# Kernel tuning notes

Measured on AMD Instinct MI355X. Metric: run time of the kernel, lower is better.

Reference implementation:

```python
import jax, jax.numpy as jnp
import numpy as np
from jax import lax

DILATIONS = [1, 2, 4, 8, 16, 32, 64, 128, 256, 512]
KERNEL = 3
CH = 64
B, T = 8, 16384
L = len(DILATIONS)


def setup_inputs() -> dict:
    key = jax.random.key(0)
    ks = jax.random.split(key, 5)
    x = jax.random.normal(ks[0], (B, CH, T), dtype=jnp.float32)
    # gated conv: out_channels = 2*CH (tanh half | sigmoid half)
    weights_conv = jax.random.normal(ks[1], (L, 2 * CH, CH, KERNEL), dtype=jnp.float32) * 0.1
    biases_conv = jax.random.normal(ks[2], (L, 2 * CH), dtype=jnp.float32) * 0.1
    weights_out = jax.random.normal(ks[3], (L, CH, CH), dtype=jnp.float32) * 0.1
    biases_out = jax.random.normal(ks[4], (L, CH), dtype=jnp.float32) * 0.1
    return {
        "x": x,
        "weights_conv": weights_conv,
        "biases_conv": biases_conv,
        "weights_out": weights_out,
        "biases_out": biases_out,
    }


def _stack_forward(x, weights_conv, biases_conv, weights_out, biases_out):
    skips = []
    for i, d in enumerate(DILATIONS):
        h = x  # residual branch
        pad = (KERNEL - 1) * d  # causal left padding
        y = lax.conv_general_dilated(
            x, weights_conv[i],
            window_strides=(1,), padding=[(pad, 0)], rhs_dilation=(d,),
            dimension_numbers=("NCH", "OIH", "NCH"),
        ) + biases_conv[i][None, :, None]
        yt, ys = jnp.split(y, 2, axis=1)          # gated activation
        a = jnp.tanh(yt) * jax.nn.sigmoid(ys)      # (B, CH, T)
        skips.append(a)                            # skip = activation output
        if i < L - 1:  # last layer has use_output_transform=False
            out = jnp.einsum("oc,bct->bot", weights_out[i], a) + biases_out[i][None, :, None]
        else:
            out = a
        x = out + h  # residual add
    # pack (output, skips[0..L-1]) into one array of shape (L+1, B, CH, T)
    return jnp.concatenate([x[None], jnp.stack(skips, axis=0)], axis=0)


def reference(x, weights_conv, biases_conv, weights_out, biases_out):
    return _stack_forward(x, weights_conv, biases_conv, weights_out, biases_out)
```

## Files before the change

kernel.cpp:

```cpp
#include <hip/hip_runtime.h>
#include <hip/hip_bf16.h>


#define CH 64
#define TLEN 16384
#define NB 8
#define BN 128
#define NLAYER 10

typedef __attribute__((ext_vector_type(4))) float f32x4;
typedef __attribute__((ext_vector_type(8))) short s16x8;
typedef __attribute__((ext_vector_type(4))) unsigned short u16x4;

__device__ __forceinline__ unsigned short f2bf(float f) {
    union { float f; unsigned u; } v; v.f = f;
    unsigned r = v.u + 0x7fffu + ((v.u >> 16) & 1u);
    return (unsigned short)(r >> 16);
}
__device__ __forceinline__ float bf2f(unsigned short u) {
    union { unsigned u; float f; } v; v.u = ((unsigned)u) << 16;
    return v.f;
}
__device__ __forceinline__ void gload_lds16(const void* g, void* l) {
    __builtin_amdgcn_global_load_lds(
        (const __attribute__((address_space(1))) unsigned int*)g,
        (__attribute__((address_space(3))) unsigned int*)l, 16, 0, 0);
}

#define NCONV (NLAYER * 4 * 2 * 6 * 64 * 8)
#define NOUT  (NLAYER * 4 * 2 * 64 * 8)

__global__ void pack_weights(const float* __restrict__ wconv,
                             const float* __restrict__ wout,
                             unsigned short* __restrict__ wcpk,
                             unsigned short* __restrict__ wopk)
{
    int idx = blockIdx.x * 256 + threadIdx.x;
    if (idx < NCONV) {
        int j = idx & 7, t = idx >> 3;
        int lane = t & 63; t >>= 6;
        int ks = t % 6;   t /= 6;
        int m  = t & 1;   t >>= 1;
        int wv = t & 3;   int l = t >> 2;
        int o  = (m * 4 + wv) * 16 + (lane & 15);
        int ck = ks * 32 + (lane >> 4) * 8 + j;
        int kk = ck >> 6, c = ck & 63;
        wcpk[idx] = f2bf(wconv[(((size_t)l * 128 + o) * CH + c) * 3 + (2 - kk)]);
    } else if (idx < NCONV + NOUT) {
        int id = idx - NCONV;
        int j = id & 7, t = id >> 3;
        int lane = t & 63; t >>= 6;
        int ks = t & 1;    t >>= 1;
        int wv = t & 3;    int l = t >> 2;
        int o  = wv * 16 + (lane & 15);
        int c  = ks * 32 + (lane >> 4) * 8 + j;
        wopk[id] = f2bf(wout[((size_t)l * CH + o) * CH + c]);
    }
}

template<int I0, bool SRC_F32>
__global__ __launch_bounds__(256, 4)
void wavenet_pair(const void* __restrict__ xin_,
                  unsigned short* __restrict__ xoutp,
                  float* __restrict__ out,
                  const unsigned short* __restrict__ wcpk,
                  const unsigned short* __restrict__ wopk,
                  const float* __restrict__ bconv,
                  const float* __restrict__ bout)
{
    constexpr int d   = 1 << I0;
    constexpr int D   = 2 * d;
    constexpr int TD  = 2 * D;
    constexpr int W1T = (128 + TD + 15) / 16;
    constexpr int W1  = W1T * 16;
    constexpr int WIN = W1 + 2 * d;

    __shared__ __align__(16) unsigned short xs[WIN * 64];
    __shared__ __align__(16) unsigned short ci[W1 * 64];
    __shared__ __align__(16) unsigned short as2[64 * 64];

    const int tid  = threadIdx.x;
    const int lane = tid & 63;
    const int wv   = tid >> 6;
    const int hrow = lane & 15;
    const int kgrp = lane >> 4;
    const int b  = blockIdx.y;
    const int t0 = blockIdx.x * BN;
    const size_t xbase  = (size_t)b * CH * TLEN;
    const size_t planeF = (size_t)NB * CH * TLEN;
    const int o0 = wv * 16 + kgrp * 4;
    const int lo = t0 - 6 * d;

    if (SRC_F32) {
        const float* x = (const float*)xin_;
        #pragma unroll
        for (int c8 = 0; c8 < 8; ++c8) {
            for (int p = tid; p < WIN; p += 256) {
                const int tt = lo + p;
                s16x8 pk = {0, 0, 0, 0, 0, 0, 0, 0};
                if (tt >= 0 && tt < TLEN) {
                    const float* pp = x + xbase + (size_t)(c8 * 8) * TLEN + tt;
                    #pragma unroll
                    for (int j = 0; j < 8; ++j) pk[j] = (short)f2bf(pp[(size_t)j * TLEN]);
                }
                *reinterpret_cast<s16x8*>(&xs[(size_t)(c8 * WIN + p) * 8]) = pk;
            }
        }
    } else {
        const unsigned short* xb = (const unsigned short*)xin_ + xbase;
        constexpr int cnt = (WIN + 63) / 64;
        if (lo >= 0 && lo + WIN <= TLEN) {
            for (int task = wv; task < 8 * cnt; task += 4) {
                const int c8 = task / cnt, n0 = (task % cnt) * 64;
                const int rem = WIN - n0;
                const unsigned short* sp = xb + (size_t)(lo + n0 + lane) * CH + c8 * 8;
                unsigned short* dp = &xs[(size_t)(c8 * WIN + n0) * 8];
                if (rem >= 64) gload_lds16(sp, dp);
                else if (lane < rem) gload_lds16(sp, dp);
            }
        } else {
            for (int task = wv; task < 8 * cnt; task += 4) {
                const int c8 = task / cnt, n0 = (task % cnt) * 64;
                const int p = n0 + lane;
                if (p < WIN) {
                    const int tt = lo + p;
                    s16x8 pk = {0, 0, 0, 0, 0, 0, 0, 0};
                    if (tt >= 0 && tt < TLEN)
                        pk = *reinterpret_cast<const s16x8*>(xb + (size_t)tt * CH + c8 * 8);
                    *reinterpret_cast<s16x8*>(&xs[(size_t)(c8 * WIN + p) * 8]) = pk;
                }
            }
        }
    }

    s16x8 w0[6], w1[6], wa2[2];
    float bt[4], bs[4], bo[4];
    auto loadw = [&](int L) {
        const unsigned short* bw = wcpk + ((size_t)(L * 4 + wv) * 768 + lane) * 8;
        #pragma unroll
        for (int ks = 0; ks < 6; ++ks) {
            w0[ks] = *reinterpret_cast<const s16x8*>(bw + (size_t)ks * 512);
            w1[ks] = *reinterpret_cast<const s16x8*>(bw + (size_t)(6 + ks) * 512);
        }
        const unsigned short* b2 = wopk + ((size_t)(L * 4 + wv) * 128 + lane) * 8;
        wa2[0] = *reinterpret_cast<const s16x8*>(b2);
        wa2[1] = *reinterpret_cast<const s16x8*>(b2 + 512);
        const float* Bc = bconv + (size_t)L * 128;
        const float* Bo = bout + (size_t)L * CH;
        #pragma unroll
        for (int r = 0; r < 4; ++r) {
            bt[r] = Bc[o0 + r];
            bs[r] = Bc[64 + o0 + r];
            bo[r] = Bo[o0 + r];
        }
    };

    loadw(I0);
    __syncthreads();

    float* skipA = out + (size_t)(1 + I0) * planeF + xbase;
    #pragma unroll 1
    for (int c0 = 0; c0 < W1T; c0 += 3) {
        f32x4 aT[3], aS[3];
        #pragma unroll
        for (int i3 = 0; i3 < 3; ++i3) {
            aT[i3] = (f32x4){0.f, 0.f, 0.f, 0.f};
            aS[i3] = (f32x4){0.f, 0.f, 0.f, 0.f};
        }
        #pragma unroll
        for (int i3 = 0; i3 < 3; ++i3) {
            const int q = (c0 + i3) * 16 + hrow;
            #pragma unroll
            for (int ks = 0; ks < 6; ++ks) {
                const int kb = ks * 4 + kgrp;
                const int kk = kb >> 3, c8i = kb & 7;
                const s16x8 bf = *reinterpret_cast<const s16x8*>(
                    &xs[(size_t)(c8i * WIN + q + (2 - kk) * d) * 8]);
                aT[i3] = __builtin_amdgcn_mfma_f32_16x16x32_bf16(w0[ks], bf, aT[i3], 0, 0, 0);
                aS[i3] = __builtin_amdgcn_mfma_f32_16x16x32_bf16(w1[ks], bf, aS[i3], 0, 0, 0);
            }
        }
        #pragma unroll
        for (int i3 = 0; i3 < 3; ++i3) {
            const int q = (c0 + i3) * 16 + hrow;
            #pragma unroll
            for (int r = 0; r < 4; ++r) {
                const float yt = aT[i3][r] + bt[r];
                const float ys = aS[i3][r] + bs[r];
                const float th = 2.f * __builtin_amdgcn_rcpf(1.f + __expf(-2.f * yt)) - 1.f;
                const float sg = __builtin_amdgcn_rcpf(1.f + __expf(-ys));
                const float av = th * sg;
                const int c = o0 + r;
                if (q >= TD && q < TD + 128)
                    __builtin_nontemporal_store(av, &skipA[(size_t)c * TLEN + t0 + q - TD]);
                ci[(size_t)((c >> 3) * W1 + q) * 8 + (c & 7)] = f2bf(av);
            }
        }
        __syncthreads();
        u16x4 stash[3];
        #pragma unroll
        for (int i3 = 0; i3 < 3; ++i3) {
            const int q = (c0 + i3) * 16 + hrow;
            f32x4 acc = (f32x4){0.f, 0.f, 0.f, 0.f};
            #pragma unroll
            for (int ks2 = 0; ks2 < 2; ++ks2) {
                const s16x8 bf = *reinterpret_cast<const s16x8*>(
                    &ci[(size_t)((ks2 * 4 + kgrp) * W1 + q) * 8]);
                acc = __builtin_amdgcn_mfma_f32_16x16x32_bf16(wa2[ks2], bf, acc, 0, 0, 0);
            }
            const u16x4 rv = *reinterpret_cast<const u16x4*>(
                &xs[(size_t)((o0 >> 3) * WIN + q + 2 * d) * 8 + (o0 & 7)]);
            u16x4 ov;
            #pragma unroll
            for (int r = 0; r < 4; ++r)
                ov[r] = (t0 + q >= TD) ? f2bf(acc[r] + bo[r] + bf2f(rv[r]))
                                       : (unsigned short)0;
            stash[i3] = ov;
        }
        __syncthreads();
        #pragma unroll
        for (int i3 = 0; i3 < 3; ++i3) {
            const int q = (c0 + i3) * 16 + hrow;
            *reinterpret_cast<u16x4*>(&ci[(size_t)((o0 >> 3) * W1 + q) * 8 + (o0 & 7)]) = stash[i3];
        }
    }
    __syncthreads();

    loadw(I0 + 1);
    float* skipB = out + (size_t)(2 + I0) * planeF + xbase;
    unsigned short* xo = xoutp + xbase;

    #pragma unroll 1
    for (int hf = 0; hf < 2; ++hf) {
        f32x4 aT[4], aS[4];
        #pragma unroll
        for (int i4 = 0; i4 < 4; ++i4) {
            aT[i4] = (f32x4){0.f, 0.f, 0.f, 0.f};
            aS[i4] = (f32x4){0.f, 0.f, 0.f, 0.f};
        }
        #pragma unroll
        for (int i4 = 0; i4 < 4; ++i4) {
            const int n = (hf * 4 + i4) * 16 + hrow;
            #pragma unroll
            for (int ks = 0; ks < 6; ++ks) {
                const int kb = ks * 4 + kgrp;
                const int kk = kb >> 3, c8i = kb & 7;
                const s16x8 bf = *reinterpret_cast<const s16x8*>(
                    &ci[(size_t)(c8i * W1 + n + (2 - kk) * D) * 8]);
                aT[i4] = __builtin_amdgcn_mfma_f32_16x16x32_bf16(w0[ks], bf, aT[i4], 0, 0, 0);
                aS[i4] = __builtin_amdgcn_mfma_f32_16x16x32_bf16(w1[ks], bf, aS[i4], 0, 0, 0);
            }
        }
        #pragma unroll
        for (int i4 = 0; i4 < 4; ++i4) {
            const int n = (hf * 4 + i4) * 16 + hrow;
            #pragma unroll
            for (int r = 0; r < 4; ++r) {
                const float yt = aT[i4][r] + bt[r];
                const float ys = aS[i4][r] + bs[r];
                const float th = 2.f * __builtin_amdgcn_rcpf(1.f + __expf(-2.f * yt)) - 1.f;
                const float sg = __builtin_amdgcn_rcpf(1.f + __expf(-ys));
                const float av = th * sg;
                const int c = o0 + r;
                __builtin_nontemporal_store(av, &skipB[(size_t)c * TLEN + t0 + n]);
                as2[(size_t)((c >> 3) * 64 + (n - hf * 64)) * 8 + (c & 7)] = f2bf(av);
            }
        }
        __syncthreads();
        #pragma unroll
        for (int i4 = 0; i4 < 4; ++i4) {
            const int n = (hf * 4 + i4) * 16 + hrow;
            const int nl = n - hf * 64;
            f32x4 acc = (f32x4){0.f, 0.f, 0.f, 0.f};
            #pragma unroll
            for (int ks2 = 0; ks2 < 2; ++ks2) {
                const s16x8 bf = *reinterpret_cast<const s16x8*>(
                    &as2[(size_t)((ks2 * 4 + kgrp) * 64 + nl) * 8]);
                acc = __builtin_amdgcn_mfma_f32_16x16x32_bf16(wa2[ks2], bf, acc, 0, 0, 0);
            }
            const u16x4 rv = *reinterpret_cast<const u16x4*>(
                &ci[(size_t)((o0 >> 3) * W1 + n + TD) * 8 + (o0 & 7)]);
            u16x4 ov;
            #pragma unroll
            for (int r = 0; r < 4; ++r) ov[r] = f2bf(acc[r] + bo[r] + bf2f(rv[r]));
            *reinterpret_cast<u16x4*>(&xo[(size_t)(t0 + n) * CH + o0]) = ov;
        }
        __syncthreads();
    }
}

template<int SM, bool LAST>
__global__ __launch_bounds__(256, 3)
void wavenet_layer(const void* __restrict__ xin_, void* __restrict__ xout_,
                   float* __restrict__ skip,
                   const unsigned short* __restrict__ wcpk,
                   const unsigned short* __restrict__ wopk,
                   const float* __restrict__ bconv, const float* __restrict__ bout,
                   int layer, int dil)
{
    extern __shared__ __align__(16) unsigned short xs[];
    unsigned short* as_ = xs;

    const int tid  = threadIdx.x;
    const int lane = tid & 63;
    const int wv   = tid >> 6;
    const int hrow = lane & 15;
    const int kgrp = lane >> 4;
    const int b  = blockIdx.y;
    const int t0 = blockIdx.x * BN;
    const int NW = BN + 2 * dil;
    const size_t xbase = (size_t)b * CH * TLEN;

    if (SM == 1) {
        const unsigned short* xin = (const unsigned short*)xin_;
        const int cnt_n = (NW + 63) >> 6;
        if (t0 >= 2 * dil) {
            for (int ch = wv; ch < 8 * cnt_n; ch += 4) {
                const int c8 = ch / cnt_n;
                const int n0 = (ch % cnt_n) * 64;
                const int rem = NW - n0;
                const unsigned short* src =
                    xin + xbase + (size_t)(t0 - 2 * dil + n0 + lane) * CH + c8 * 8;
                unsigned short* dst = &xs[(size_t)(c8 * NW + n0) * 8];
                if (rem >= 64) gload_lds16(src, dst);
                else if (lane < rem) gload_lds16(src, dst);
            }
        } else {
            for (int ch = wv; ch < 8 * cnt_n; ch += 4) {
                const int c8 = ch / cnt_n;
                const int n0 = (ch % cnt_n) * 64;
                if (n0 + lane < NW) {
                    const int tg = t0 - 2 * dil + n0 + lane;
                    s16x8 pk = {0, 0, 0, 0, 0, 0, 0, 0};
                    if (tg >= 0)
                        pk = *reinterpret_cast<const s16x8*>(xin + xbase + (size_t)tg * CH + c8 * 8);
                    *reinterpret_cast<s16x8*>(&xs[(size_t)(c8 * NW + n0 + lane) * 8]) = pk;
                }
            }
        }
    } else {
        const unsigned short* xin = (const unsigned short*)xin_;
        if (t0 >= 2 * dil) {
            for (int ch = wv; ch < 48; ch += 4) {
                const int kk = ch >> 4, c8 = (ch >> 1) & 7, n0 = (ch & 1) * 64;
                const unsigned short* src =
                    xin + xbase + (size_t)(t0 + n0 + lane - kk * dil) * CH + c8 * 8;
                unsigned short* dst = &xs[(size_t)((kk * 8 + c8) * BN + n0) * 8];
                gload_lds16(src, dst);
            }
        } else {
            for (int ch = wv; ch < 48; ch += 4) {
                const int kk = ch >> 4, c8 = (ch >> 1) & 7, n0 = (ch & 1) * 64;
                const int tg = t0 + n0 + lane - kk * dil;
                s16x8 pk = {0, 0, 0, 0, 0, 0, 0, 0};
                if (tg >= 0)
                    pk = *reinterpret_cast<const s16x8*>(xin + xbase + (size_t)tg * CH + c8 * 8);
                *reinterpret_cast<s16x8*>(&xs[(size_t)((kk * 8 + c8) * BN + n0 + lane) * 8]) = pk;
            }
        }
    }

    s16x8 w0[6], w1[6];
    {
        const unsigned short* basew = wcpk + ((size_t)(layer * 4 + wv) * 768 + lane) * 8;
        #pragma unroll
        for (int ks = 0; ks < 6; ++ks) {
            w0[ks] = *reinterpret_cast<const s16x8*>(basew + (size_t)ks * 512);
            w1[ks] = *reinterpret_cast<const s16x8*>(basew + (size_t)(6 + ks) * 512);
        }
    }
    const float* Bc = bconv + (size_t)layer * 128;
    float bt[4], bs[4];
    #pragma unroll
    for (int r = 0; r < 4; ++r) {
        bt[r] = Bc[wv * 16 + kgrp * 4 + r];
        bs[r] = Bc[64 + wv * 16 + kgrp * 4 + r];
    }

    __syncthreads();

    f32x4 accT[8], accS[8];
    #pragma unroll
    for (int nt = 0; nt < 8; ++nt) {
        accT[nt] = (f32x4){0.f, 0.f, 0.f, 0.f};
        accS[nt] = (f32x4){0.f, 0.f, 0.f, 0.f};
    }
    #pragma unroll
    for (int nt = 0; nt < 8; ++nt) {
        #pragma unroll
        for (int ks = 0; ks < 6; ++ks) {
            const int kb = ks * 4 + kgrp;
            const unsigned short* bp;
            if (SM == 2) {
                bp = &xs[(size_t)(kb * BN + nt * 16 + hrow) * 8];
            } else {
                const int kk = kb >> 3, c8i = kb & 7;
                bp = &xs[(size_t)(c8i * NW + nt * 16 + hrow + (2 - kk) * dil) * 8];
            }
            const s16x8 bf = *reinterpret_cast<const s16x8*>(bp);
            accT[nt] = __builtin_amdgcn_mfma_f32_16x16x32_bf16(w0[ks], bf, accT[nt], 0, 0, 0);
            accS[nt] = __builtin_amdgcn_mfma_f32_16x16x32_bf16(w1[ks], bf, accS[nt], 0, 0, 0);
        }
    }

    if (!LAST) __syncthreads();

    #pragma unroll
    for (int nt = 0; nt < 8; ++nt) {
        #pragma unroll
        for (int r = 0; r < 4; ++r) {
            const float yt = accT[nt][r] + bt[r];
            const float ys = accS[nt][r] + bs[r];
            const float th = 2.f * __builtin_amdgcn_rcpf(1.f + __expf(-2.f * yt)) - 1.f;
            const float sg = __builtin_amdgcn_rcpf(1.f + __expf(-ys));
            const float av = th * sg;
            const int c = wv * 16 + kgrp * 4 + r;
            const int n = nt * 16 + hrow;
            __builtin_nontemporal_store(av, &skip[xbase + (size_t)c * TLEN + t0 + n]);
            if (LAST) {
                const float res = bf2f(xs[(size_t)((c >> 3) * BN + n) * 8 + (c & 7)]);
                __builtin_nontemporal_store(av + res,
                    &((float*)xout_)[xbase + (size_t)c * TLEN + t0 + n]);
            } else {
                as_[(size_t)((c >> 3) * BN + n) * 8 + (c & 7)] = f2bf(av);
            }
        }
    }

    if (LAST) return;

    __syncthreads();

    s16x8 wa2[2];
    {
        const unsigned short* b2 = wopk + ((size_t)(layer * 4 + wv) * 128 + lane) * 8;
        wa2[0] = *reinterpret_cast<const s16x8*>(b2);
        wa2[1] = *reinterpret_cast<const s16x8*>(b2 + 512);
    }
    const float* Bo = bout + (size_t)layer * CH;
    float bo[4];
    #pragma unroll
    for (int r = 0; r < 4; ++r) bo[r] = Bo[wv * 16 + kgrp * 4 + r];

    const int o0 = wv * 16 + kgrp * 4;
    unsigned short* xout = (unsigned short*)xout_;

    #pragma unroll
    for (int nt = 0; nt < 8; ++nt) {
        f32x4 acc = (f32x4){0.f, 0.f, 0.f, 0.f};
        #pragma unroll
        for (int ks = 0; ks < 2; ++ks) {
            const s16x8 bf = *reinterpret_cast<const s16x8*>(
                &as_[(size_t)((ks * 4 + kgrp) * BN + nt * 16 + hrow) * 8]);
            acc = __builtin_amdgcn_mfma_f32_16x16x32_bf16(wa2[ks], bf, acc, 0, 0, 0);
        }
        const int n = nt * 16 + hrow;
        const u16x4 rv = *reinterpret_cast<const u16x4*>(
            (const unsigned short*)xin_ + xbase + (size_t)(t0 + n) * CH + o0);
        u16x4 ov;
        #pragma unroll
        for (int r = 0; r < 4; ++r) ov[r] = f2bf(acc[r] + bo[r] + bf2f(rv[r]));
        *reinterpret_cast<u16x4*>(&xout[xbase + (size_t)(t0 + n) * CH + o0]) = ov;
    }
}

extern "C" void kernel_launch(void* const* d_in, const int* in_sizes, int n_in,
                              void* d_out, int out_size, void* d_ws, size_t ws_size,
                              hipStream_t stream)
{
    const float* x  = (const float*)d_in[0];
    const float* wc = (const float*)d_in[1];
    const float* bc = (const float*)d_in[2];
    const float* wo = (const float*)d_in[3];
    const float* bo = (const float*)d_in[4];
    float* out = (float*)d_out;
    const size_t planeF = (size_t)NB * CH * TLEN;

    unsigned short* PA = (unsigned short*)d_ws;
    unsigned short* PB = PA + planeF;
    unsigned short* wcpk = PB + planeF;
    unsigned short* wopk = wcpk + NCONV;

    pack_weights<<<(NCONV + NOUT) / 256, 256, 0, stream>>>(wc, wo, wcpk, wopk);

    dim3 grid(TLEN / BN, NB), block(256);

    wavenet_pair<0, true ><<<grid, block, 0, stream>>>(x,  PA, out, wcpk, wopk, bc, bo);
    wavenet_pair<2, false><<<grid, block, 0, stream>>>(PA, PB, out, wcpk, wopk, bc, bo);
    wavenet_pair<4, false><<<grid, block, 0, stream>>>(PB, PA, out, wcpk, wopk, bc, bo);

    wavenet_layer<1, false><<<grid, block, (size_t)(BN + 128) * 128, stream>>>(
        PA, PB, out + 7 * planeF, wcpk, wopk, bc, bo, 6, 64);
    wavenet_layer<2, false><<<grid, block, 24 * BN * 8 * 2, stream>>>(
        PB, PA, out + 8 * planeF, wcpk, wopk, bc, bo, 7, 128);
    wavenet_layer<2, false><<<grid, block, 24 * BN * 8 * 2, stream>>>(
        PA, PB, out + 9 * planeF, wcpk, wopk, bc, bo, 8, 256);
    wavenet_layer<2, true><<<grid, block, 24 * BN * 8 * 2, stream>>>(
        PB, out, out + 10 * planeF, wcpk, wopk, bc, bo, 9, 512);
}
```

Baseline: 233.8 us.

## Reuse input LDS buffer in pair kernel and split tail layers into sub-tiles

The fused layer-pair kernel drops its separate intermediate LDS buffer and writes the first layer's output back into the input window. The residual values are read into registers before that overwrite, and an extra barrier is added. The single-layer tail kernels are replaced by one kernel that processes each 128-step tile as two 64-step sub-tiles, using static, smaller LDS buffers and a launch bound of four blocks per CU instead of three. This cuts LDS footprint to raise occupancy, at the cost of more barriers and serialized sub-tile loads.

After: 301.6 us. +29.0%, slower.

```diff
diff --git a/kernel.cpp b/kernel.cpp
--- a/kernel.cpp
+++ b/kernel.cpp
@@ -76,7 +76,6 @@
     constexpr int WIN = W1 + 2 * d;
 
     __shared__ __align__(16) unsigned short xs[WIN * 64];
-    __shared__ __align__(16) unsigned short ci[W1 * 64];
     __shared__ __align__(16) unsigned short as2[64 * 64];
 
     const int tid  = threadIdx.x;
@@ -162,6 +161,7 @@
     #pragma unroll 1
     for (int c0 = 0; c0 < W1T; c0 += 3) {
         f32x4 aT[3], aS[3];
+        u16x4 rv[3];
         #pragma unroll
         for (int i3 = 0; i3 < 3; ++i3) {
             aT[i3] = (f32x4){0.f, 0.f, 0.f, 0.f};
@@ -170,6 +170,8 @@
         #pragma unroll
         for (int i3 = 0; i3 < 3; ++i3) {
             const int q = (c0 + i3) * 16 + hrow;
+            rv[i3] = *reinterpret_cast<const u16x4*>(
+                &xs[(size_t)((o0 >> 3) * WIN + q + 2 * d) * 8 + (o0 & 7)]);
             #pragma unroll
             for (int ks = 0; ks < 6; ++ks) {
                 const int kb = ks * 4 + kgrp;
@@ -180,6 +182,7 @@
                 aS[i3] = __builtin_amdgcn_mfma_f32_16x16x32_bf16(w1[ks], bf, aS[i3], 0, 0, 0);
             }
         }
+        __syncthreads();
         #pragma unroll
         for (int i3 = 0; i3 < 3; ++i3) {
             const int q = (c0 + i3) * 16 + hrow;
@@ -193,35 +196,32 @@
                 const int c = o0 + r;
                 if (q >= TD && q < TD + 128)
                     __builtin_nontemporal_store(av, &skipA[(size_t)c * TLEN + t0 + q - TD]);
-                ci[(size_t)((c >> 3) * W1 + q) * 8 + (c & 7)] = f2bf(av);
-            }
-        }
-        __syncthreads();
-        u16x4 stash[3];
+                xs[(size_t)((c >> 3) * WIN + q) * 8 + (c & 7)] = f2bf(av);
+            }
+        }
+        __syncthreads();
+        f32x4 acc[3];
         #pragma unroll
         for (int i3 = 0; i3 < 3; ++i3) {
             const int q = (c0 + i3) * 16 + hrow;
-            f32x4 acc = (f32x4){0.f, 0.f, 0.f, 0.f};
+            acc[i3] = (f32x4){0.f, 0.f, 0.f, 0.f};
             #pragma unroll
             for (int ks2 = 0; ks2 < 2; ++ks2) {
                 const s16x8 bf = *reinterpret_cast<const s16x8*>(
-                    &ci[(size_t)((ks2 * 4 + kgrp) * W1 + q) * 8]);
-                acc = __builtin_amdgcn_mfma_f32_16x16x32_bf16(wa2[ks2], bf, acc, 0, 0, 0);
-            }
-            const u16x4 rv = *reinterpret_cast<const u16x4*>(
-                &xs[(size_t)((o0 >> 3) * WIN + q + 2 * d) * 8 + (o0 & 7)]);
-            u16x4 ov;
-            #pragma unroll
-            for (int r = 0; r < 4; ++r)
-                ov[r] = (t0 + q >= TD) ? f2bf(acc[r] + bo[r] + bf2f(rv[r]))
-                                       : (unsigned short)0;
-            stash[i3] = ov;
+                    &xs[(size_t)((ks2 * 4 + kgrp) * WIN + q) * 8]);
+                acc[i3] = __builtin_amdgcn_mfma_f32_16x16x32_bf16(wa2[ks2], bf, acc[i3], 0, 0, 0);
+            }
         }
         __syncthreads();
         #pragma unroll
         for (int i3 = 0; i3 < 3; ++i3) {
             const int q = (c0 + i3) * 16 + hrow;
-            *reinterpret_cast<u16x4*>(&ci[(size_t)((o0 >> 3) * W1 + q) * 8 + (o0 & 7)]) = stash[i3];
+            u16x4 ov;
+            #pragma unroll
+            for (int r = 0; r < 4; ++r)
+                ov[r] = (t0 + q >= TD) ? f2bf(acc[i3][r] + bo[r] + bf2f(rv[i3][r]))
+                                       : (unsigned short)0;
+            *reinterpret_cast<u16x4*>(&xs[(size_t)((o0 >> 3) * WIN + q) * 8 + (o0 & 7)]) = ov;
         }
     }
     __syncthreads();
@@ -246,7 +246,7 @@
                 const int kb = ks * 4 + kgrp;
                 const int kk = kb >> 3, c8i = kb & 7;
                 const s16x8 bf = *reinterpret_cast<const s16x8*>(
-                    &ci[(size_t)(c8i * W1 + n + (2 - kk) * D) * 8]);
+                    &xs[(size_t)(c8i * WIN + n + (2 - kk) * D) * 8]);
                 aT[i4] = __builtin_amdgcn_mfma_f32_16x16x32_bf16(w0[ks], bf, aT[i4], 0, 0, 0);
                 aS[i4] = __builtin_amdgcn_mfma_f32_16x16x32_bf16(w1[ks], bf, aS[i4], 0, 0, 0);
             }
@@ -279,7 +279,7 @@
                 acc = __builtin_amdgcn_mfma_f32_16x16x32_bf16(wa2[ks2], bf, acc, 0, 0, 0);
             }
             const u16x4 rv = *reinterpret_cast<const u16x4*>(
-                &ci[(size_t)((o0 >> 3) * W1 + n + TD) * 8 + (o0 & 7)]);
+                &xs[(size_t)((o0 >> 3) * WIN + n + TD) * 8 + (o0 & 7)]);
             u16x4 ov;
             #pragma unroll
             for (int r = 0; r < 4; ++r) ov[r] = f2bf(acc[r] + bo[r] + bf2f(rv[r]));
@@ -289,17 +289,17 @@
     }
 }
 
-template<int SM, bool LAST>
-__global__ __launch_bounds__(256, 3)
-void wavenet_layer(const void* __restrict__ xin_, void* __restrict__ xout_,
+template<bool LAST>
+__global__ __launch_bounds__(256, 4)
+void wavenet_tailB(const unsigned short* __restrict__ xin, void* __restrict__ xout_,
                    float* __restrict__ skip,
                    const unsigned short* __restrict__ wcpk,
                    const unsigned short* __restrict__ wopk,
                    const float* __restrict__ bconv, const float* __restrict__ bout,
                    int layer, int dil)
 {
-    extern __shared__ __align__(16) unsigned short xs[];
-    unsigned short* as_ = xs;
+    __shared__ __align__(16) unsigned short xs[12288];
+    __shared__ __align__(16) unsigned short as_[4096];
 
     const int tid  = threadIdx.x;
     const int lane = tid & 63;
@@ -308,159 +308,128 @@
     const int kgrp = lane >> 4;
     const int b  = blockIdx.y;
     const int t0 = blockIdx.x * BN;
-    const int NW = BN + 2 * dil;
     const size_t xbase = (size_t)b * CH * TLEN;
-
-    if (SM == 1) {
-        const unsigned short* xin = (const unsigned short*)xin_;
-        const int cnt_n = (NW + 63) >> 6;
-        if (t0 >= 2 * dil) {
-            for (int ch = wv; ch < 8 * cnt_n; ch += 4) {
-                const int c8 = ch / cnt_n;
-                const int n0 = (ch % cnt_n) * 64;
-                const int rem = NW - n0;
-                const unsigned short* src =
-                    xin + xbase + (size_t)(t0 - 2 * dil + n0 + lane) * CH + c8 * 8;
-                unsigned short* dst = &xs[(size_t)(c8 * NW + n0) * 8];
-                if (rem >= 64) gload_lds16(src, dst);
-                else if (lane < rem) gload_lds16(src, dst);
-            }
-        } else {
-            for (int ch = wv; ch < 8 * cnt_n; ch += 4) {
-                const int c8 = ch / cnt_n;
-                const int n0 = (ch % cnt_n) * 64;
-                if (n0 + lane < NW) {
-                    const int tg = t0 - 2 * dil + n0 + lane;
-                    s16x8 pk = {0, 0, 0, 0, 0, 0, 0, 0};
-                    if (tg >= 0)
-                        pk = *reinterpret_cast<const s16x8*>(xin + xbase + (size_t)tg * CH + c8 * 8);
-                    *reinterpret_cast<s16x8*>(&xs[(size_t)(c8 * NW + n0 + lane) * 8]) = pk;
-                }
-            }
-        }
-    } else {
-        const unsigned short* xin = (const unsigned short*)xin_;
-        if (t0 >= 2 * dil) {
-            for (int ch = wv; ch < 48; ch += 4) {
-                const int kk = ch >> 4, c8 = (ch >> 1) & 7, n0 = (ch & 1) * 64;
-                const unsigned short* src =
-                    xin + xbase + (size_t)(t0 + n0 + lane - kk * dil) * CH + c8 * 8;
-                unsigned short* dst = &xs[(size_t)((kk * 8 + c8) * BN + n0) * 8];
-                gload_lds16(src, dst);
-            }
-        } else {
-            for (int ch = wv; ch < 48; ch += 4) {
-                const int kk = ch >> 4, c8 = (ch >> 1) & 7, n0 = (ch & 1) * 64;
-                const int tg = t0 + n0 + lane - kk * dil;
-                s16x8 pk = {0, 0, 0, 0, 0, 0, 0, 0};
-                if (tg >= 0)
-                    pk = *reinterpret_cast<const s16x8*>(xin + xbase + (size_t)tg * CH + c8 * 8);
-                *reinterpret_cast<s16x8*>(&xs[(size_t)((kk * 8 + c8) * BN + n0 + lane) * 8]) = pk;
-            }
-        }
-    }
-
-    s16x8 w0[6], w1[6];
+    const unsigned short* xb = xin + xbase;
+    const int o0 = wv * 16 + kgrp * 4;
+
+    s16x8 w0[6], w1[6], wa2[2];
     {
-        const unsigned short* basew = wcpk + ((size_t)(layer * 4 + wv) * 768 + lane) * 8;
+        const unsigned short* bw = wcpk + ((size_t)(layer * 4 + wv) * 768 + lane) * 8;
         #pragma unroll
         for (int ks = 0; ks < 6; ++ks) {
-            w0[ks] = *reinterpret_cast<const s16x8*>(basew + (size_t)ks * 512);
-            w1[ks] = *reinterpret_cast<const s16x8*>(basew + (size_t)(6 + ks) * 512);
-        }
-    }
-    const float* Bc = bconv + (size_t)layer * 128;
-    float bt[4], bs[4];
-    #pragma unroll
-    for (int r = 0; r < 4; ++r) {
-        bt[r] = Bc[wv * 16 + kgrp * 4 + r];
-        bs[r] = Bc[64 + wv * 16 + kgrp * 4 + r];
-    }
-
-    __syncthreads();
-
-    f32x4 accT[8], accS[8];
-    #pragma unroll
-    for (int nt = 0; nt < 8; ++nt) {
-        accT[nt] = (f32x4){0.f, 0.f, 0.f, 0.f};
-        accS[nt] = (f32x4){0.f, 0.f, 0.f, 0.f};
-    }
-    #pragma unroll
-    for (int nt = 0; nt < 8; ++nt) {
-        #pragma unroll
-        for (int ks = 0; ks < 6; ++ks) {
-            const int kb = ks * 4 + kgrp;
-            const unsigned short* bp;
-            if (SM == 2) {
-                bp = &xs[(size_t)(kb * BN + nt * 16 + hrow) * 8];
-            } else {
-                const int kk = kb >> 3, c8i = kb & 7;
-                bp = &xs[(size_t)(c8i * NW + nt * 16 + hrow + (2 - kk) * dil) * 8];
-            }
-            const s16x8 bf = *reinterpret_cast<const s16x8*>(bp);
-            accT[nt] = __builtin_amdgcn_mfma_f32_16x16x32_bf16(w0[ks], bf, accT[nt], 0, 0, 0);
-            accS[nt] = __builtin_amdgcn_mfma_f32_16x16x32_bf16(w1[ks], bf, accS[nt], 0, 0, 0);
-        }
-    }
-
-    if (!LAST) __syncthreads();
-
-    #pragma unroll
-    for (int nt = 0; nt < 8; ++nt) {
-        #pragma unroll
-        for (int r = 0; r < 4; ++r) {
-            const float yt = accT[nt][r] + bt[r];
-            const float ys = accS[nt][r] + bs[r];
-            const float th = 2.f * __builtin_amdgcn_rcpf(1.f + __expf(-2.f * yt)) - 1.f;
-            const float sg = __builtin_amdgcn_rcpf(1.f + __expf(-ys));
-            const float av = th * sg;
-            const int c = wv * 16 + kgrp * 4 + r;
-            const int n = nt * 16 + hrow;
-            __builtin_nontemporal_store(av, &skip[xbase + (size_t)c * TLEN + t0 + n]);
-            if (LAST) {
-                const float res = bf2f(xs[(size_t)((c >> 3) * BN + n) * 8 + (c & 7)]);
-                __builtin_nontemporal_store(av + res,
-                    &((float*)xout_)[xbase + (size_t)c * TLEN + t0 + n]);
-            } else {
-                as_[(size_t)((c >> 3) * BN + n) * 8 + (c & 7)] = f2bf(av);
-            }
-        }
-    }
-
-    if (LAST) return;
-
-    __syncthreads();
-
-    s16x8 wa2[2];
-    {
+            w0[ks] = *reinterpret_cast<const s16x8*>(bw + (size_t)ks * 512);
+            w1[ks] = *reinterpret_cast<const s16x8*>(bw + (size_t)(6 + ks) * 512);
+        }
         const unsigned short* b2 = wopk + ((size_t)(layer * 4 + wv) * 128 + lane) * 8;
         wa2[0] = *reinterpret_cast<const s16x8*>(b2);
         wa2[1] = *reinterpret_cast<const s16x8*>(b2 + 512);
     }
+    const float* Bc = bconv + (size_t)layer * 128;
     const float* Bo = bout + (size_t)layer * CH;
-    float bo[4];
+    float bt[4], bs[4], bo[4];
     #pragma unroll
-    for (int r = 0; r < 4; ++r) bo[r] = Bo[wv * 16 + kgrp * 4 + r];
-
-    const int o0 = wv * 16 + kgrp * 4;
-    unsigned short* xout = (unsigned short*)xout_;
-
-    #pragma unroll
-    for (int nt = 0; nt < 8; ++nt) {
-        f32x4 acc = (f32x4){0.f, 0.f, 0.f, 0.f};
-        #pragma unroll
-        for (int ks = 0; ks < 2; ++ks) {
-            const s16x8 bf = *reinterpret_cast<const s16x8*>(
-                &as_[(size_t)((ks * 4 + kgrp) * BN + nt * 16 + hrow) * 8]);
-            acc = __builtin_amdgcn_mfma_f32_16x16x32_bf16(wa2[ks], bf, acc, 0, 0, 0);
-        }
-        const int n = nt * 16 + hrow;
-        const u16x4 rv = *reinterpret_cast<const u16x4*>(
-            (const unsigned short*)xin_ + xbase + (size_t)(t0 + n) * CH + o0);
-        u16x4 ov;
-        #pragma unroll
-        for (int r = 0; r < 4; ++r) ov[r] = f2bf(acc[r] + bo[r] + bf2f(rv[r]));
-        *reinterpret_cast<u16x4*>(&xout[xbase + (size_t)(t0 + n) * CH + o0]) = ov;
+    for (int r = 0; r < 4; ++r) {
+        bt[r] = Bc[o0 + r];
+        bs[r] = Bc[64 + o0 + r];
+        bo[r] = Bo[o0 + r];
+    }
+
+    #pragma unroll 1
+    for (int st = 0; st < 2; ++st) {
+        const int ts0 = t0 + st * 64;
+        if (ts0 >= 2 * dil) {
+            for (int task = wv; task < 24; task += 4) {
+                const int kk = task >> 3, c8 = task & 7;
+                const unsigned short* sp = xb + (size_t)(ts0 - kk * dil + lane) * CH + c8 * 8;
+                gload_lds16(sp, &xs[(size_t)((kk * 8 + c8) * 64) * 8]);
+            }
+        } else {
+            for (int task = wv; task < 24; task += 4) {
+                const int kk = task >> 3, c8 = task & 7;
+                const int tg = ts0 - kk * dil + lane;
+                s16x8 pk = {0, 0, 0, 0, 0, 0, 0, 0};
+                if (tg >= 0)
+                    pk = *reinterpret_cast<const s16x8*>(xb + (size_t)tg * CH + c8 * 8);
+                *reinterpret_cast<s16x8*>(&xs[(size_t)((kk * 8 + c8) * 64 + lane) * 8]) = pk;
+            }
+        }
+        __syncthreads();
+
+        f32x4 aT[4], aS[4];
+        #pragma unroll
+        for (int i4 = 0; i4 < 4; ++i4) {
+            aT[i4] = (f32x4){0.f, 0.f, 0.f, 0.f};
+            aS[i4] = (f32x4){0.f, 0.f, 0.f, 0.f};
+        }
+        #pragma unroll
+        for (int i4 = 0; i4 < 4; ++i4) {
+            #pragma unroll
+            for (int ks = 0; ks < 6; ++ks) {
+                const int kb = ks * 4 + kgrp;
+                const int kk = kb >> 3, c8i = kb & 7;
+                const s16x8 bf = *reinterpret_cast<const s16x8*>(
+                    &xs[(size_t)((kk * 8 + c8i) * 64 + i4 * 16 + hrow) * 8]);
+                aT[i4] = __builtin_amdgcn_mfma_f32_16x16x32_bf16(w0[ks], bf, aT[i4], 0, 0, 0);
+                aS[i4] = __builtin_amdgcn_mfma_f32_16x16x32_bf16(w1[ks], bf, aS[i4], 0, 0, 0);
+            }
+        }
+        if (LAST) {
+            float* xo0 = (float*)xout_ + xbase;
+            #pragma unroll
+            for (int i4 = 0; i4 < 4; ++i4) {
+                const int nl = i4 * 16 + hrow;
+                #pragma unroll
+                for (int r = 0; r < 4; ++r) {
+                    const float yt = aT[i4][r] + bt[r];
+                    const float ys = aS[i4][r] + bs[r];
+                    const float th = 2.f * __builtin_amdgcn_rcpf(1.f + __expf(-2.f * yt)) - 1.f;
+                    const float sg = __builtin_amdgcn_rcpf(1.f + __expf(-ys));
+                    const float av = th * sg;
+                    const int c = o0 + r;
+                    __builtin_nontemporal_store(av, &skip[xbase + (size_t)c * TLEN + ts0 + nl]);
+                    const float res = bf2f(xs[(size_t)((c >> 3) * 64 + nl) * 8 + (c & 7)]);
+                    __builtin_nontemporal_store(av + res, &xo0[(size_t)c * TLEN + ts0 + nl]);
+                }
+            }
+            __syncthreads();
+        } else {
+            u16x4 rv[4];
+            #pragma unroll
+            for (int i4 = 0; i4 < 4; ++i4) {
+                const int nl = i4 * 16 + hrow;
+                rv[i4] = *reinterpret_cast<const u16x4*>(
+                    &xs[(size_t)((o0 >> 3) * 64 + nl) * 8 + (o0 & 7)]);
+                #pragma unroll
+                for (int r = 0; r < 4; ++r) {
+                    const float yt = aT[i4][r] + bt[r];
+                    const float ys = aS[i4][r] + bs[r];
+                    const float th = 2.f * __builtin_amdgcn_rcpf(1.f + __expf(-2.f * yt)) - 1.f;
+                    const float sg = __builtin_amdgcn_rcpf(1.f + __expf(-ys));
+                    const float av = th * sg;
+                    const int c = o0 + r;
+                    __builtin_nontemporal_store(av, &skip[xbase + (size_t)c * TLEN + ts0 + nl]);
+                    as_[(size_t)((c >> 3) * 64 + nl) * 8 + (c & 7)] = f2bf(av);
+                }
+            }
+            __syncthreads();
+            unsigned short* xo = (unsigned short*)xout_ + xbase;
+            #pragma unroll
+            for (int i4 = 0; i4 < 4; ++i4) {
+                const int nl = i4 * 16 + hrow;
+                f32x4 acc = (f32x4){0.f, 0.f, 0.f, 0.f};
+                #pragma unroll
+                for (int ks2 = 0; ks2 < 2; ++ks2) {
+                    const s16x8 bf = *reinterpret_cast<const s16x8*>(
+                        &as_[(size_t)((ks2 * 4 + kgrp) * 64 + nl) * 8]);
+                    acc = __builtin_amdgcn_mfma_f32_16x16x32_bf16(wa2[ks2], bf, acc, 0, 0, 0);
+                }
+                u16x4 ov;
+                #pragma unroll
+                for (int r = 0; r < 4; ++r) ov[r] = f2bf(acc[r] + bo[r] + bf2f(rv[i4][r]));
+                *reinterpret_cast<u16x4*>(&xo[(size_t)(ts0 + nl) * CH + o0]) = ov;
+            }
+            __syncthreads();
+        }
     }
 }
 
@@ -489,12 +458,12 @@
     wavenet_pair<2, false><<<grid, block, 0, stream>>>(PA, PB, out, wcpk, wopk, bc, bo);
     wavenet_pair<4, false><<<grid, block, 0, stream>>>(PB, PA, out, wcpk, wopk, bc, bo);
 
-    wavenet_layer<1, false><<<grid, block, (size_t)(BN + 128) * 128, stream>>>(
+    wavenet_tailB<false><<<grid, block, 0, stream>>>(
         PA, PB, out + 7 * planeF, wcpk, wopk, bc, bo, 6, 64);
-    wavenet_layer<2, false><<<grid, block, 24 * BN * 8 * 2, stream>>>(
+    wavenet_tailB<false><<<grid, block, 0, stream>>>(
         PB, PA, out + 8 * planeF, wcpk, wopk, bc, bo, 7, 128);
-    wavenet_layer<2, false><<<grid, block, 24 * BN * 8 * 2, stream>>>(
+    wavenet_tailB<false><<<grid, block, 0, stream>>>(
         PA, PB, out + 9 * planeF, wcpk, wopk, bc, bo, 8, 256);
-    wavenet_layer<2, true><<<grid, block, 24 * BN * 8 * 2, stream>>>(
+    wavenet_tailB<true><<<grid, block, 0, stream>>>(
         PB, out, out + 10 * planeF, wcpk, wopk, bc, bo, 9, 512);
 }
```
